# Kernel tuning notes

Hardware: AMD Instinct MI355X
Metric: run time of the kernel (lower is better)

## Reference

```python
import jax, jax.numpy as jnp
import numpy as np
from jax import lax

T, R, W, F_CWT, E, H, HG, NC, K = 16, 200, 50, 32, 128, 256, 256, 2, 20


def _make_wavelets():
    t = np.linspace(-1.0, 1.0, W)
    w0 = 6.0
    freqs = np.linspace(1.0, W / 2.0, F_CWT)
    wr = np.zeros((F_CWT, 1, W), np.float32)
    wi = np.zeros((F_CWT, 1, W), np.float32)
    for i, s in enumerate(freqs):
        norm = s ** (-0.5) * np.pi ** (-0.25)
        ts = t / s
        psi = norm * np.exp(1j * w0 * ts) * np.exp(-0.5 * ts ** 2)
        wr[i, 0] = psi.real.astype(np.float32)
        wi[i, 0] = psi.imag.astype(np.float32)
    return jnp.asarray(wr), jnp.asarray(wi)


def setup_inputs() -> dict:
    key = jax.random.key(0)
    ks = jax.random.split(key, 20)
    wr, wi = _make_wavelets()
    s = 0.05
    inp = {
        "time_windows": jax.random.normal(ks[0], (T, R, W), jnp.float32),
        "wav_real": wr, "wav_imag": wi,
        "conv1_w": jax.random.normal(ks[1], (16, 1, 3, 3), jnp.float32) * s,
        "conv1_b": jnp.zeros((16,), jnp.float32),
        "bn1_g": jnp.ones((16,), jnp.float32), "bn1_b": jnp.zeros((16,), jnp.float32),
        "conv2_w": jax.random.normal(ks[2], (32, 16, 3, 3), jnp.float32) * s,
        "conv2_b": jnp.zeros((32,), jnp.float32),
        "bn2_g": jnp.ones((32,), jnp.float32), "bn2_b": jnp.zeros((32,), jnp.float32),
        "fc_w": jax.random.normal(ks[3], (E, 32), jnp.float32) * s,
        "fc_b": jnp.zeros((E,), jnp.float32),
        "q_w": jax.random.normal(ks[4], (E, E), jnp.float32) * s,
        "q_b": jnp.zeros((E,), jnp.float32),
        "k_w": jax.random.normal(ks[5], (E, E), jnp.float32) * s,
        "k_b": jnp.zeros((E,), jnp.float32),
        "gcn1_w": jax.random.normal(ks[6], (E, H), jnp.float32) * s,
        "gcn1_b": jnp.zeros((H,), jnp.float32),
        "gcn2_w": jax.random.normal(ks[7], (H, H), jnp.float32) * s,
        "gcn2_b": jnp.zeros((H,), jnp.float32),
        "gru_wih": jax.random.normal(ks[8], (3 * HG, H), jnp.float32) * s,
        "gru_whh": jax.random.normal(ks[9], (3 * HG, HG), jnp.float32) * s,
        "gru_bih": jnp.zeros((3 * HG,), jnp.float32),
        "gru_bhh": jnp.zeros((3 * HG,), jnp.float32),
        "cls_w": jax.random.normal(ks[10], (NC, HG), jnp.float32) * s,
        "cls_b": jnp.zeros((NC,), jnp.float32),
    }
    return inp


def _conv_bn_relu_pool(x, w, b, g, beta):
    # conv2d k3 pad1, training-mode BN, relu, maxpool2 (floor)
    x = lax.conv_general_dilated(x, w, (1, 1), ((1, 1), (1, 1)),
                                 dimension_numbers=("NCHW", "OIHW", "NCHW"))
    x = x + b[None, :, None, None]
    mu = x.mean((0, 2, 3), keepdims=True)
    var = x.var((0, 2, 3), keepdims=True)
    x = (x - mu) * lax.rsqrt(var + 1e-5) * g[None, :, None, None] + beta[None, :, None, None]
    x = jax.nn.relu(x)
    return lax.reduce_window(x, -jnp.inf, lax.max, (1, 1, 2, 2), (1, 1, 2, 2), "VALID")


def _forward(time_windows, wav_real, wav_imag, conv1_w, conv1_b, bn1_g, bn1_b,
             conv2_w, conv2_b, bn2_g, bn2_b, fc_w, fc_b, q_w, q_b, k_w, k_b,
             gcn1_w, gcn1_b, gcn2_w, gcn2_b, gru_wih, gru_whh, gru_bih, gru_bhh,
             cls_w, cls_b):
    N = T * R
    x = time_windows.reshape(N, 1, W)
    pl = (W - 1) // 2
    pr = (W - 1) - pl  # torch padding='same' (extra on right)
    re = lax.conv_general_dilated(x, wav_real, (1,), [(pl, pr)],
                                  dimension_numbers=("NCH", "OIH", "NCH"))
    im = lax.conv_general_dilated(x, wav_imag, (1,), [(pl, pr)],
                                  dimension_numbers=("NCH", "OIH", "NCH"))
    scal = jnp.sqrt(re * re + im * im)              # [N, F_CWT, W]

    h = scal[:, None]                               # [N,1,F,W]
    h = _conv_bn_relu_pool(h, conv1_w, conv1_b, bn1_g, bn1_b)
    h = _conv_bn_relu_pool(h, conv2_w, conv2_b, bn2_g, bn2_b)
    pooled = h.mean((2, 3))                         # adaptive avg pool -> [N,32]
    emb = pooled @ fc_w.T + fc_b                    # [N,E]
    emb = emb.reshape(T, R, E)

    # sparse-attention graph generation (per window, vectorized over T)
    Q = emb @ q_w.T + q_b
    Kp = emb @ k_w.T + k_b
    attn = jnp.einsum("tre,tse->trs", Q, Kp) / (E ** 0.5)
    attn = jax.nn.leaky_relu(attn, 0.2)
    _, idx = lax.top_k(attn, K)                     # [T,R,K]
    mask = jnp.zeros_like(attn).at[
        jnp.arange(T)[:, None, None], jnp.arange(R)[None, :, None], idx].set(1.0)
    masked = attn * mask
    masked = jnp.where(masked == 0.0, -1e9, masked)
    adj = jax.nn.softmax(masked, axis=-1)           # [T,R,R] row-stochastic, topk-sparse

    # GCNConv x2 with edge weights (PyG gcn_norm: remaining self-loops weight 1,
    ii = jnp.arange(R)
    diag = adj[:, ii, ii]
    adj_sl = adj.at[:, ii, ii].set(jnp.where(diag == 0.0, 1.0, diag))
    Bm = jnp.swapaxes(adj_sl, 1, 2)
    deg = Bm.sum(-1)
    dinv = jnp.where(deg > 0, deg, 1.0) ** -0.5
    An = dinv[:, :, None] * Bm * dinv[:, None, :]   # [T,R,R]
    g = jax.nn.relu(jnp.einsum("trs,tsh->trh", An, emb @ gcn1_w) + gcn1_b)
    g = jax.nn.relu(jnp.einsum("trs,tsh->trh", An, g @ gcn2_w) + gcn2_b)
    g_emb = g.mean(1)                               # [T,H]

    # GRU over the T graph embeddings (batch 1, gate order r,z,n)
    def step(hprev, xt):
        gi = xt @ gru_wih.T + gru_bih
        gh = hprev @ gru_whh.T + gru_bhh
        ir, iz, inn = jnp.split(gi, 3)
        hr, hz, hn = jnp.split(gh, 3)
        r = jax.nn.sigmoid(ir + hr)
        z = jax.nn.sigmoid(iz + hz)
        n = jnp.tanh(inn + r * hn)
        return (1.0 - z) * n + z * hprev, None

    hT, _ = lax.scan(step, jnp.zeros((HG,), emb.dtype), g_emb)
    pred = (hT @ cls_w.T + cls_b)[None]             # [1,NC]

    edge_var = jnp.mean(jnp.var(adj, axis=0, ddof=1))
    avg_adj = adj.mean(0)[None]                     # [1,R,R]
    return pred, avg_adj, edge_var


def reference(time_windows, wav_real, wav_imag, conv1_w, conv1_b, bn1_g, bn1_b,
              conv2_w, conv2_b, bn2_g, bn2_b, fc_w, fc_b, q_w, q_b, k_w, k_b,
              gcn1_w, gcn1_b, gcn2_w, gcn2_b, gru_wih, gru_whh, gru_bih, gru_bhh,
              cls_w, cls_b):
    return _forward(time_windows, wav_real, wav_imag, conv1_w, conv1_b, bn1_g, bn1_b,
                    conv2_w, conv2_b, bn2_g, bn2_b, fc_w, fc_b, q_w, q_b, k_w, k_b,
                    gcn1_w, gcn1_b, gcn2_w, gcn2_b, gru_wih, gru_whh, gru_bih, gru_bhh,
                    cls_w, cls_b)
```

## Files before the change

### kernel.cpp

```cpp
#include <hip/hip_runtime.h>
#include <cfloat>
#include <cmath>

#define T_ 16
#define R_ 200
#define W_ 50
#define FCWT 32
#define E_ 128
#define K_ 20
#define N_ 3200
#define GRU_BLOCKS 6

__device__ __forceinline__ void waveReduce2(float& a, float& b) {
#pragma unroll
    for (int o = 32; o > 0; o >>= 1) {
        a += __shfl_down(a, o, 64);
        b += __shfl_down(b, o, 64);
    }
}

__global__ __launch_bounds__(256) void cwt_conv1_stats_kernel(const float* __restrict__ x,
                                                              const float* __restrict__ wr,
                                                              const float* __restrict__ wi,
                                                              const float* __restrict__ w1,
                                                              const float* __restrict__ b1,
                                                              float* __restrict__ scal,
                                                              double* __restrict__ psum,
                                                              double* __restrict__ psq) {
    int n = blockIdx.x, tid = threadIdx.x;
    __shared__ float sxp[112];
    __shared__ float swr[FCWT * W_];
    __shared__ float swi[FCWT * W_];
    __shared__ float P1[34 * 52];
    __shared__ float ls[256], lq[256];
    if (tid < 112) sxp[tid] = (tid >= 24 && tid < 74) ? x[n * 50 + (tid - 24)] : 0.f;
    for (int idx = tid; idx < FCWT * W_; idx += 256) { swr[idx] = wr[idx]; swi[idx] = wi[idx]; }
    for (int idx = tid; idx < 34 * 52; idx += 256) P1[idx] = 0.f;
    __syncthreads();
    if (tid < 64) {
        int f = tid >> 1, i0 = (tid & 1) * 25;
        float xw[25], ar[25], ai[25];
#pragma unroll
        for (int d = 0; d < 25; ++d) { xw[d] = sxp[i0 + d]; ar[d] = 0.f; ai[d] = 0.f; }
        const float* wrf = &swr[f * 50];
        const float* wif = &swi[f * 50];
        for (int j = 0; j < 50; ++j) {
            float wrv = wrf[j], wiv = wif[j];
#pragma unroll
            for (int d = 0; d < 25; ++d) { ar[d] += xw[d] * wrv; ai[d] += xw[d] * wiv; }
            float xnew = sxp[i0 + j + 25];
#pragma unroll
            for (int d = 0; d < 24; ++d) xw[d] = xw[d + 1];
            xw[24] = xnew;
        }
#pragma unroll
        for (int d = 0; d < 25; ++d) {
            float v = sqrtf(ar[d] * ar[d] + ai[d] * ai[d]);
            P1[(f + 1) * 52 + (i0 + d + 1)] = v;
        }
    }
    __syncthreads();
    for (int idx = tid; idx < 1600; idx += 256) {
        int ff = idx / 50, ii = idx % 50;
        scal[n * 1600 + idx] = P1[(ff + 1) * 52 + ii + 1];
    }
    int c = tid & 15, pg = tid >> 4;
    float wv[9];
#pragma unroll
    for (int k = 0; k < 9; ++k) wv[k] = w1[c * 9 + k];
    float bias = b1[c];
    const float* r0p = &P1[(2 * pg + 0) * 52];
    const float* r1p = &P1[(2 * pg + 1) * 52];
    const float* r2p = &P1[(2 * pg + 2) * 52];
    const float* r3p = &P1[(2 * pg + 3) * 52];
    float c0[4], c1[4];
    c0[0] = r0p[0]; c0[1] = r1p[0]; c0[2] = r2p[0]; c0[3] = r3p[0];
    c1[0] = r0p[1]; c1[1] = r1p[1]; c1[2] = r2p[1]; c1[3] = r3p[1];
    float s = 0.f, q = 0.f;
    for (int xx = 0; xx < 50; ++xx) {
        float c2[4];
        c2[0] = r0p[xx + 2]; c2[1] = r1p[xx + 2]; c2[2] = r2p[xx + 2]; c2[3] = r3p[xx + 2];
        float v0 = bias + c0[0] * wv[0] + c1[0] * wv[1] + c2[0] * wv[2]
                        + c0[1] * wv[3] + c1[1] * wv[4] + c2[1] * wv[5]
                        + c0[2] * wv[6] + c1[2] * wv[7] + c2[2] * wv[8];
        float v1 = bias + c0[1] * wv[0] + c1[1] * wv[1] + c2[1] * wv[2]
                        + c0[2] * wv[3] + c1[2] * wv[4] + c2[2] * wv[5]
                        + c0[3] * wv[6] + c1[3] * wv[7] + c2[3] * wv[8];
        s += v0 + v1; q += v0 * v0 + v1 * v1;
#pragma unroll
        for (int rr = 0; rr < 4; ++rr) { c0[rr] = c1[rr]; c1[rr] = c2[rr]; }
    }
    ls[tid] = s; lq[tid] = q;
    __syncthreads();
    if (tid < 16) {
        float ss = 0.f, qq = 0.f;
        for (int g = 0; g < 16; ++g) { ss += ls[tid + 16 * g]; qq += lq[tid + 16 * g]; }
        psum[n * 16 + tid] = (double)ss;
        psq[n * 16 + tid] = (double)qq;
    }
}

__global__ __launch_bounds__(256) void bn_finalize_kernel(const double* __restrict__ psum,
                                                          const double* __restrict__ psq,
                                                          const float* __restrict__ g,
                                                          const float* __restrict__ beta,
                                                          float* __restrict__ scale,
                                                          float* __restrict__ shift,
                                                          int C, double inv_count) {
    int c = blockIdx.x, tid = threadIdx.x;
    double s = 0.0, q = 0.0;
    for (int n = tid; n < N_; n += 256) { s += psum[n * C + c]; q += psq[n * C + c]; }
#pragma unroll
    for (int o = 32; o > 0; o >>= 1) { s += __shfl_down(s, o, 64); q += __shfl_down(q, o, 64); }
    __shared__ double sa[4], sb[4];
    int lane = tid & 63, wid = tid >> 6;
    if (lane == 0) { sa[wid] = s; sb[wid] = q; }
    __syncthreads();
    if (tid == 0) {
        s = sa[0] + sa[1] + sa[2] + sa[3];
        q = sb[0] + sb[1] + sb[2] + sb[3];
        double mu = s * inv_count;
        double var = q * inv_count - mu * mu;
        double rstd = 1.0 / sqrt(var + 1e-5);
        double gg = (double)g[c];
        scale[c] = (float)(gg * rstd);
        shift[c] = (float)((double)beta[c] - mu * rstd * gg);
    }
}

__global__ __launch_bounds__(256) void conv1_norm_pool_kernel(const float* __restrict__ scal,
                                                              const float* __restrict__ w1,
                                                              const float* __restrict__ b1,
                                                              const float* __restrict__ scale,
                                                              const float* __restrict__ shift,
                                                              float* __restrict__ pooled1) {
    int n = blockIdx.x, tid = threadIdx.x;
    __shared__ float P1[34 * 52];
    __shared__ float outb[6400];
    for (int idx = tid; idx < 34 * 52; idx += 256) {
        int yy = idx / 52, xx = idx % 52;
        float v = 0.f;
        if (yy >= 1 && yy <= 32 && xx >= 1 && xx <= 50)
            v = scal[n * 1600 + (yy - 1) * 50 + (xx - 1)];
        P1[idx] = v;
    }
    __syncthreads();
    int c = tid & 15, py = tid >> 4;
    float wv[9];
#pragma unroll
    for (int k = 0; k < 9; ++k) wv[k] = w1[c * 9 + k];
    float bias = b1[c], sc = scale[c], sh = shift[c];
    const float* r0p = &P1[(2 * py + 0) * 52];
    const float* r1p = &P1[(2 * py + 1) * 52];
    const float* r2p = &P1[(2 * py + 2) * 52];
    const float* r3p = &P1[(2 * py + 3) * 52];
    float c0[4], c1[4];
    c0[0] = r0p[0]; c0[1] = r1p[0]; c0[2] = r2p[0]; c0[3] = r3p[0];
    c1[0] = r0p[1]; c1[1] = r1p[1]; c1[2] = r2p[1]; c1[3] = r3p[1];
    float pmax = -FLT_MAX;
    for (int xx = 0; xx < 50; ++xx) {
        float c2[4];
        c2[0] = r0p[xx + 2]; c2[1] = r1p[xx + 2]; c2[2] = r2p[xx + 2]; c2[3] = r3p[xx + 2];
        float v0 = bias + c0[0] * wv[0] + c1[0] * wv[1] + c2[0] * wv[2]
                        + c0[1] * wv[3] + c1[1] * wv[4] + c2[1] * wv[5]
                        + c0[2] * wv[6] + c1[2] * wv[7] + c2[2] * wv[8];
        float v1 = bias + c0[1] * wv[0] + c1[1] * wv[1] + c2[1] * wv[2]
                        + c0[2] * wv[3] + c1[2] * wv[4] + c2[2] * wv[5]
                        + c0[3] * wv[6] + c1[3] * wv[7] + c2[3] * wv[8];
        float m2 = fmaxf(v0 * sc + sh, v1 * sc + sh);
        if ((xx & 1) == 0) pmax = m2;
        else outb[(c * 16 + py) * 25 + (xx >> 1)] = fmaxf(fmaxf(pmax, m2), 0.f);
#pragma unroll
        for (int rr = 0; rr < 4; ++rr) { c0[rr] = c1[rr]; c1[rr] = c2[rr]; }
    }
    __syncthreads();
    for (int idx = tid; idx < 6400; idx += 256)
        pooled1[(size_t)n * 6400 + idx] = outb[idx];
}

__global__ __launch_bounds__(256) void conv2_compute_kernel(const float* __restrict__ pooled1,
                                                            const float* __restrict__ w2,
                                                            const float* __restrict__ b2,
                                                            float* __restrict__ mm,
                                                            double* __restrict__ psum,
                                                            double* __restrict__ psq,
                                                            int store_min) {
    int n = blockIdx.x, tid = threadIdx.x;
    __shared__ float P2[16 * 18 * 28];
    __shared__ float swT[144 * 32];
    __shared__ float ls[256], lq[256];
    for (int idx = tid; idx < 16 * 18 * 28; idx += 256) {
        int ci = idx / 504, rem = idx % 504, yy = rem / 28, xx = rem % 28;
        float v = 0.f;
        if (yy >= 1 && yy <= 16 && xx >= 1 && xx <= 25)
            v = pooled1[((size_t)n * 16 + ci) * 400 + (yy - 1) * 25 + (xx - 1)];
        P2[idx] = v;
    }
    for (int idx = tid; idx < 4608; idx += 256) {
        int co = idx / 144, r = idx % 144;
        swT[r * 32 + co] = w2[idx];
    }
    __syncthreads();
    int co = tid & 31, pg = tid >> 5;
    float bias = b2[co];
    float acc0[25], acc1[25];
#pragma unroll
    for (int cv = 0; cv < 25; ++cv) { acc0[cv] = bias; acc1[cv] = bias; }
    for (int ci = 0; ci < 16; ++ci) {
        const float* wb = &swT[ci * 288 + co];
        float w[9];
#pragma unroll
        for (int k = 0; k < 9; ++k) w[k] = wb[k * 32];
        const float* base = &P2[ci * 504 + (2 * pg) * 28];
#pragma unroll
        for (int iy = 0; iy < 4; ++iy) {
            float r[28];
            const float4* rp = (const float4*)(base + iy * 28);
#pragma unroll
            for (int m = 0; m < 7; ++m) {
                float4 v4 = rp[m];
                r[4 * m] = v4.x; r[4 * m + 1] = v4.y; r[4 * m + 2] = v4.z; r[4 * m + 3] = v4.w;
            }
            if (iy < 3) {
                int kb = iy * 3;
#pragma unroll
                for (int cv = 0; cv < 25; ++cv)
                    acc0[cv] += r[cv] * w[kb] + r[cv + 1] * w[kb + 1] + r[cv + 2] * w[kb + 2];
            }
            if (iy >= 1) {
                int kb = (iy - 1) * 3;
#pragma unroll
                for (int cv = 0; cv < 25; ++cv)
                    acc1[cv] += r[cv] * w[kb] + r[cv + 1] * w[kb + 1] + r[cv + 2] * w[kb + 2];
            }
        }
    }
    float s = 0.f, q = 0.f;
#pragma unroll
    for (int cv = 0; cv < 25; ++cv) {
        s += acc0[cv] + acc1[cv];
        q += acc0[cv] * acc0[cv] + acc1[cv] * acc1[cv];
    }
    int stride = store_min ? 64 : 32;
#pragma unroll
    for (int pc = 0; pc < 12; ++pc) {
        float v00 = acc0[2 * pc], v01 = acc0[2 * pc + 1];
        float v10 = acc1[2 * pc], v11 = acc1[2 * pc + 1];
        float mx = fmaxf(fmaxf(v00, v01), fmaxf(v10, v11));
        int cell = pg * 12 + pc;
        mm[((size_t)n * 96 + cell) * stride + co] = mx;
        if (store_min) {
            float mn = fminf(fminf(v00, v01), fminf(v10, v11));
            mm[((size_t)n * 96 + cell) * 64 + 32 + co] = mn;
        }
    }
    ls[tid] = s; lq[tid] = q;
    __syncthreads();
    if (tid < 32) {
        float ss = 0.f, qq = 0.f;
        for (int g2 = 0; g2 < 8; ++g2) { ss += ls[tid + 32 * g2]; qq += lq[tid + 32 * g2]; }
        psum[n * 32 + tid] = (double)ss;
        psq[n * 32 + tid] = (double)qq;
    }
}

__global__ __launch_bounds__(256) void pool_mean_kernel(const float* __restrict__ mm,
                                                        const float* __restrict__ scale,
                                                        const float* __restrict__ shift,
                                                        float* __restrict__ pm,
                                                        int store_min) {
    int n = blockIdx.x, tid = threadIdx.x;
    int co = tid & 31, grp = tid >> 5;
    float sc = scale[co], sh = shift[co];
    int stride = store_min ? 64 : 32;
    float acc = 0.f;
    for (int j = 0; j < 12; ++j) {
        int cell = grp * 12 + j;
        float v;
        if (store_min && sc < 0.f) {
            float mn = mm[((size_t)n * 96 + cell) * 64 + 32 + co];
            v = mn * sc + sh;
        } else {
            float mx = mm[((size_t)n * 96 + cell) * stride + co];
            v = mx * sc + sh;
        }
        acc += fmaxf(v, 0.f);
    }
    __shared__ float red[256];
    red[tid] = acc;
    __syncthreads();
    if (tid < 32) {
        float t = 0.f;
        for (int g = 0; g < 8; ++g) t += red[co + 32 * g];
        pm[n * 32 + co] = t * (1.f / 96.f);
    }
}

__global__ __launch_bounds__(128) void fc_kernel(const float* __restrict__ pm,
                                                 const float* __restrict__ fc_w,
                                                 const float* __restrict__ fc_b,
                                                 float* __restrict__ emb) {
    int n = blockIdx.x, e = threadIdx.x;
    __shared__ float sp[32];
    if (e < 32) sp[e] = pm[n * 32 + e];
    __syncthreads();
    const float* w = fc_w + e * 32;
    float acc = fc_b[e];
    for (int c = 0; c < 32; ++c) acc += sp[c] * w[c];
    emb[n * 128 + e] = acc;
}

__global__ __launch_bounds__(128) void qk_kernel(const float* __restrict__ emb,
                                                 const float* __restrict__ q_w,
                                                 const float* __restrict__ q_b,
                                                 const float* __restrict__ k_w,
                                                 const float* __restrict__ k_b,
                                                 float* __restrict__ Q,
                                                 float* __restrict__ Kp) {
    int n = blockIdx.x, e = threadIdx.x;
    const float* w = (blockIdx.y == 0) ? q_w : k_w;
    const float* b = (blockIdx.y == 0) ? q_b : k_b;
    float* out = (blockIdx.y == 0) ? Q : Kp;
    __shared__ float se[128];
    se[e] = emb[n * 128 + e];
    __syncthreads();
    const float* wr = w + e * 128;
    float acc = b[e];
    for (int k = 0; k < 128; ++k) acc += se[k] * wr[k];
    out[n * 128 + e] = acc;
}

__global__ __launch_bounds__(256) void attn_kernel(const float* __restrict__ Q,
                                                   const float* __restrict__ Kp,
                                                   float* __restrict__ attn) {
    int r = blockIdx.x, t = blockIdx.y, tid = threadIdx.x;
    __shared__ float sq[128];
    if (tid < 128) sq[tid] = Q[(t * 200 + r) * 128 + tid];
    __syncthreads();
    if (tid < 200) {
        const float4* kp4 = (const float4*)(Kp + (size_t)(t * 200 + tid) * 128);
        float acc = 0.f;
#pragma unroll 8
        for (int e4 = 0; e4 < 32; ++e4) {
            float4 k4 = kp4[e4];
            acc += sq[e4 * 4 + 0] * k4.x + sq[e4 * 4 + 1] * k4.y +
                   sq[e4 * 4 + 2] * k4.z + sq[e4 * 4 + 3] * k4.w;
        }
        acc = acc / 11.313708498984761f;
        acc = (acc >= 0.f) ? acc : 0.2f * acc;
        attn[(size_t)(t * 200 + r) * 200 + tid] = acc;
    }
}

__global__ __launch_bounds__(64) void topk_softmax_kernel(const float* __restrict__ attn,
                                                          float* __restrict__ adj) {
    int row = blockIdx.x;
    int lane = threadIdx.x;
    const float* a = attn + (size_t)row * 200;
    float v[4], w[4];
#pragma unroll
    for (int j = 0; j < 4; ++j) {
        int i = lane + 64 * j;
        float x = (i < 200) ? a[i] : -FLT_MAX;
        v[j] = x; w[j] = x;
    }
    unsigned sel = 0;
    for (int it = 0; it < K_; ++it) {
        float best = -FLT_MAX; int bidx = 0x7fffffff;
#pragma unroll
        for (int j = 0; j < 4; ++j) {
            int i = lane + 64 * j;
            if (w[j] > best || (w[j] == best && i < bidx)) { best = w[j]; bidx = i; }
        }
#pragma unroll
        for (int off = 32; off > 0; off >>= 1) {
            float ob = __shfl_down(best, off, 64);
            int oi = __shfl_down(bidx, off, 64);
            if (ob > best || (ob == best && oi < bidx)) { best = ob; bidx = oi; }
        }
        bidx = __shfl(bidx, 0, 64);
        if ((bidx & 63) == lane) { int j = bidx >> 6; w[j] = -FLT_MAX; sel |= (1u << j); }
    }
    float mv[4]; float m = -FLT_MAX;
#pragma unroll
    for (int j = 0; j < 4; ++j) {
        int i = lane + 64 * j;
        float x = -1e9f;
        if (i < 200 && ((sel >> j) & 1u)) x = (v[j] == 0.f) ? -1e9f : v[j];
        mv[j] = x; m = fmaxf(m, x);
    }
#pragma unroll
    for (int off = 32; off > 0; off >>= 1) m = fmaxf(m, __shfl_xor(m, off, 64));
    float s = 0.f; float e[4];
#pragma unroll
    for (int j = 0; j < 4; ++j) {
        int i = lane + 64 * j;
        e[j] = (i < 200) ? expf(mv[j] - m) : 0.f;
        s += e[j];
    }
#pragma unroll
    for (int off = 32; off > 0; off >>= 1) s += __shfl_xor(s, off, 64);
    float inv = 1.f / s;
#pragma unroll
    for (int j = 0; j < 4; ++j) {
        int i = lane + 64 * j;
        if (i < 200) adj[(size_t)row * 200 + i] = e[j] * inv;
    }
}

__global__ __launch_bounds__(256) void deg_kernel(const float* __restrict__ adj,
                                                  float* __restrict__ dinv) {
    int t = blockIdx.x, tid = threadIdx.x;
    if (tid < 200) {
        float acc = 0.f;
        for (int s = 0; s < 200; ++s) {
            float v = adj[(size_t)(t * 200 + s) * 200 + tid];
            if (s == tid) v = (v == 0.f) ? 1.f : v;
            acc += v;
        }
        float d = (acc > 0.f) ? acc : 1.f;
        dinv[t * 200 + tid] = 1.f / sqrtf(d);
    }
}

__global__ __launch_bounds__(256) void an_tile_kernel(const float* __restrict__ adj,
                                                      const float* __restrict__ dinv,
                                                      float* __restrict__ An) {
    int t = blockIdx.y;
    int tr = blockIdx.x >> 2, tc = blockIdx.x & 3;
    int r0 = tr * 50, s0 = tc * 50;
    int tid = threadIdx.x;
    __shared__ float Tt[50 * 51];
    __shared__ float dr[50], ds[50];
    for (int idx = tid; idx < 2500; idx += 256) {
        int a = idx / 50, b = idx % 50;
        Tt[a * 51 + b] = adj[(size_t)(t * 200 + s0 + a) * 200 + r0 + b];
    }
    if (tid < 50) dr[tid] = dinv[t * 200 + r0 + tid];
    else if (tid >= 64 && tid < 114) ds[tid - 64] = dinv[t * 200 + s0 + (tid - 64)];
    __syncthreads();
    for (int idx = tid; idx < 2500; idx += 256) {
        int rl = idx / 50, sl = idx % 50;
        float v = Tt[sl * 51 + rl];
        if (r0 + rl == s0 + sl) v = (v == 0.f) ? 1.f : v;
        An[(size_t)(t * 200 + r0 + rl) * 200 + s0 + sl] = dr[rl] * v * ds[sl];
    }
}

__global__ __launch_bounds__(256) void linear8_kernel(const float* __restrict__ in,
                                                      const float* __restrict__ w,
                                                      float* __restrict__ out, int IN) {
    int n0 = blockIdx.x * 8, h = threadIdx.x;
    __shared__ float sin_[8 * 256];
    for (int idx = h; idx < 8 * IN; idx += 256) sin_[idx] = in[(size_t)n0 * IN + idx];
    __syncthreads();
    float acc[8];
#pragma unroll
    for (int m = 0; m < 8; ++m) acc[m] = 0.f;
    for (int k = 0; k < IN; ++k) {
        float wv = w[k * 256 + h];
#pragma unroll
        for (int m = 0; m < 8; ++m) acc[m] += sin_[m * IN + k] * wv;
    }
#pragma unroll
    for (int m = 0; m < 8; ++m) out[(size_t)(n0 + m) * 256 + h] = acc[m];
}

__global__ __launch_bounds__(256) void gcn_agg_kernel(const float* __restrict__ An,
                                                      const float* __restrict__ X,
                                                      const float* __restrict__ b,
                                                      float* __restrict__ out) {
    int t = blockIdx.y, r0 = blockIdx.x * 8, h = threadIdx.x;
    __shared__ float sa[8 * 200];
    for (int idx = h; idx < 1600; idx += 256)
        sa[idx] = An[(size_t)(t * 200 + r0) * 200 + idx];
    __syncthreads();
    const float* Xt = X + (size_t)t * 200 * 256;
    float acc[8];
#pragma unroll
    for (int m = 0; m < 8; ++m) acc[m] = 0.f;
    for (int s = 0; s < 200; ++s) {
        float xv = Xt[s * 256 + h];
#pragma unroll
        for (int m = 0; m < 8; ++m) acc[m] += sa[m * 200 + s] * xv;
    }
    float bb = b[h];
#pragma unroll
    for (int m = 0; m < 8; ++m)
        out[(size_t)(t * 200 + r0 + m) * 256 + h] = fmaxf(acc[m] + bb, 0.f);
}

__global__ __launch_bounds__(256) void gemb_kernel(const float* __restrict__ g2,
                                                   float* __restrict__ g_emb) {
    int t = blockIdx.x, h = threadIdx.x;
    float acc = 0.f;
    for (int r = 0; r < 200; ++r) acc += g2[(size_t)(t * 200 + r) * 256 + h];
    g_emb[t * 256 + h] = acc * (1.f / 200.f);
}

__global__ __launch_bounds__(256) void transpose_768x256_kernel(const float* __restrict__ in,
                                                                float* __restrict__ outT) {
    int gid = blockIdx.x * 256 + threadIdx.x;
    int k = gid / 768, j = gid % 768;
    outT[gid] = in[j * 256 + k];
}

__global__ __launch_bounds__(768) void gi_kernel(const float* __restrict__ g_emb,
                                                 const float* __restrict__ wihT,
                                                 const float* __restrict__ bih,
                                                 float* __restrict__ GI) {
    int t = blockIdx.x, j = threadIdx.x;
    __shared__ float sg[256];
    if (j < 256) sg[j] = g_emb[t * 256 + j];
    __syncthreads();
    float acc = bih[j];
    for (int k = 0; k < 256; ++k) acc += sg[k] * wihT[k * 768 + j];
    GI[t * 768 + j] = acc;
}

__global__ __launch_bounds__(256) void gru_cls_kernel(const float* __restrict__ GI,
                                                      const float* __restrict__ whhT,
                                                      const float* __restrict__ bhh,
                                                      const float* __restrict__ cls_w,
                                                      const float* __restrict__ cls_b,
                                                      float* __restrict__ GH,
                                                      int* __restrict__ flags,
                                                      float* __restrict__ out) {
    int b = blockIdx.x, tid = threadIdx.x;
    int jl = tid & 127;
    int kc = tid >> 7;
    int j = b * 128 + jl;
    float wreg[128];
#pragma unroll 16
    for (int k = 0; k < 128; ++k)
        wreg[k] = whhT[(size_t)(kc * 128 + k) * 768 + j];
    __shared__ float hcur[256];
    __shared__ float part[256];
    __shared__ float s0[4], s1[4];
    hcur[tid] = 0.f;
    __syncthreads();
    for (int st = 0; st < 16; ++st) {
        float p = 0.f;
        const float* hb = &hcur[kc * 128];
#pragma unroll 16
        for (int k = 0; k < 128; ++k) p += hb[k] * wreg[k];
        part[tid] = p;
        __syncthreads();
        if (tid < 128) {
            GH[st * 768 + b * 128 + tid] = part[tid] + part[tid + 128];
        }
        __threadfence();
        __syncthreads();
        if (tid == 0)
            __hip_atomic_store(&flags[b], st + 1, __ATOMIC_RELEASE, __HIP_MEMORY_SCOPE_AGENT);
        for (int bb = 0; bb < GRU_BLOCKS; ++bb) {
            while (__hip_atomic_load(&flags[bb], __ATOMIC_ACQUIRE, __HIP_MEMORY_SCOPE_AGENT) <= st)
                __builtin_amdgcn_s_sleep(2);
        }
        float ghr = GH[st * 768 + tid]       + bhh[tid];
        float ghz = GH[st * 768 + 256 + tid] + bhh[256 + tid];
        float ghn = GH[st * 768 + 512 + tid] + bhh[512 + tid];
        float gir = GI[st * 768 + tid];
        float giz = GI[st * 768 + 256 + tid];
        float gin = GI[st * 768 + 512 + tid];
        float r = 1.f / (1.f + expf(-(gir + ghr)));
        float z = 1.f / (1.f + expf(-(giz + ghz)));
        float nn = tanhf(gin + r * ghn);
        float hnew = (1.f - z) * nn + z * hcur[tid];
        __syncthreads();
        hcur[tid] = hnew;
        __syncthreads();
    }
    if (b == 0) {
        float v0 = hcur[tid] * cls_w[tid];
        float v1 = hcur[tid] * cls_w[256 + tid];
        waveReduce2(v0, v1);
        int lane = tid & 63, wid = tid >> 6;
        if (lane == 0) { s0[wid] = v0; s1[wid] = v1; }
        __syncthreads();
        if (tid == 0) {
            out[0] = s0[0] + s0[1] + s0[2] + s0[3] + cls_b[0];
            out[1] = s1[0] + s1[1] + s1[2] + s1[3] + cls_b[1];
        }
    }
}

__global__ __launch_bounds__(256) void edge_kernel(const float* __restrict__ adj,
                                                   float* __restrict__ out) {
    int gid = blockIdx.x * 256 + threadIdx.x;
    float var = 0.f;
    if (gid < 40000) {
        float v[16]; float s = 0.f;
#pragma unroll
        for (int t = 0; t < 16; ++t) { v[t] = adj[t * 40000 + gid]; s += v[t]; }
        float mean = s * (1.f / 16.f);
        float q = 0.f;
#pragma unroll
        for (int t = 0; t < 16; ++t) { float d = v[t] - mean; q += d * d; }
        var = q * (1.f / 15.f);
        out[2 + gid] = mean;
    }
    float dummy = 0.f;
    waveReduce2(var, dummy);
    __shared__ float sa[4];
    int lane = threadIdx.x & 63, wid = threadIdx.x >> 6;
    if (lane == 0) sa[wid] = var;
    __syncthreads();
    if (threadIdx.x == 0) {
        float bs = sa[0] + sa[1] + sa[2] + sa[3];
        atomicAdd(&out[40002], bs * (1.f / 40000.f));
    }
}

extern "C" void kernel_launch(void* const* d_in, const int* in_sizes, int n_in,
                              void* d_out, int out_size, void* d_ws, size_t ws_size,
                              hipStream_t stream) {
    const float* tw      = (const float*)d_in[0];
    const float* wav_r   = (const float*)d_in[1];
    const float* wav_i   = (const float*)d_in[2];
    const float* conv1_w = (const float*)d_in[3];
    const float* conv1_b = (const float*)d_in[4];
    const float* bn1_g   = (const float*)d_in[5];
    const float* bn1_b   = (const float*)d_in[6];
    const float* conv2_w = (const float*)d_in[7];
    const float* conv2_b = (const float*)d_in[8];
    const float* bn2_g   = (const float*)d_in[9];
    const float* bn2_b   = (const float*)d_in[10];
    const float* fc_w    = (const float*)d_in[11];
    const float* fc_b    = (const float*)d_in[12];
    const float* q_w     = (const float*)d_in[13];
    const float* q_b     = (const float*)d_in[14];
    const float* k_w     = (const float*)d_in[15];
    const float* k_b     = (const float*)d_in[16];
    const float* gcn1_w  = (const float*)d_in[17];
    const float* gcn1_b  = (const float*)d_in[18];
    const float* gcn2_w  = (const float*)d_in[19];
    const float* gcn2_b  = (const float*)d_in[20];
    const float* gru_wih = (const float*)d_in[21];
    const float* gru_whh = (const float*)d_in[22];
    const float* gru_bih = (const float*)d_in[23];
    const float* gru_bhh = (const float*)d_in[24];
    const float* cls_w   = (const float*)d_in[25];
    const float* cls_b   = (const float*)d_in[26];
    float* out = (float*)d_out;
    (void)in_sizes; (void)n_in; (void)out_size;

    const size_t POOLED1_B = (size_t)N_ * 16 * 16 * 25 * 4;
    const size_t SCALU_B   = (size_t)N_ * 1600 * 4;
    const size_t MM_FULL_B = (size_t)N_ * 96 * 64 * 4;
    const size_t MM_MAX_B  = (size_t)N_ * 96 * 32 * 4;
    const size_t P1S_B     = (size_t)N_ * 16 * 8;
    const size_t P2S_B     = (size_t)N_ * 32 * 8;
    const size_t WT_B      = (size_t)768 * 256 * 4;
    size_t fixed = POOLED1_B + SCALU_B + 2 * P1S_B + 2 * P2S_B + 2 * WT_B + 8 * 256 + 65536;
    int store_min = (ws_size >= fixed + MM_FULL_B) ? 1 : 0;
    const size_t MM_B = store_min ? MM_FULL_B : MM_MAX_B;

    size_t off = 0;
    char* Wb = (char*)d_ws;
    auto take = [&](size_t bytes) -> char* {
        char* p = Wb + off;
        off += (bytes + 255) & ~(size_t)255;
        return p;
    };
    float* pooled1 = (float*)take(POOLED1_B);
    char*  scalU   = take(SCALU_B);
    char*  mmU     = take(MM_B);
    double* p1sum = (double*)take(P1S_B);
    double* p1sq  = (double*)take(P1S_B);
    double* p2sum = (double*)take(P2S_B);
    double* p2sq  = (double*)take(P2S_B);
    float* scale1 = (float*)take(64 * 4);
    float* shift1 = (float*)take(64 * 4);
    float* scale2 = (float*)take(64 * 4);
    float* shift2 = (float*)take(64 * 4);
    float* wihT   = (float*)take(WT_B);
    float* whhT   = (float*)take(WT_B);
    float* dinv   = (float*)take((size_t)T_ * 200 * 4);
    float* GH     = (float*)take((size_t)16 * 768 * 4);
    int*   flags  = (int*)take(256);

    float* scal = (float*)scalU;
    float* pm   = (float*)(scalU + 0);
    float* emb  = (float*)(scalU + 409600);
    float* Q    = (float*)(scalU + 409600 + 1638400);
    float* Kp   = (float*)(scalU + 409600 + 2 * 1638400);

    float* mm   = (float*)mmU;
    size_t moff = 0;
    auto mtake = [&](size_t bytes) -> float* {
        float* p = (float*)(mmU + moff);
        moff += (bytes + 255) & ~(size_t)255;
        return p;
    };
    float* attn  = mtake((size_t)T_ * 200 * 200 * 4);
    float* adj   = mtake((size_t)T_ * 200 * 200 * 4);
    float* An    = mtake((size_t)T_ * 200 * 200 * 4);
    float* X1    = mtake((size_t)N_ * 256 * 4);
    float* g1    = mtake((size_t)N_ * 256 * 4);
    float* X2    = mtake((size_t)N_ * 256 * 4);
    float* g2    = mtake((size_t)N_ * 256 * 4);
    float* g_emb = mtake((size_t)T_ * 256 * 4);
    float* GI    = mtake((size_t)T_ * 768 * 4);

    transpose_768x256_kernel<<<768, 256, 0, stream>>>(gru_wih, wihT);
    transpose_768x256_kernel<<<768, 256, 0, stream>>>(gru_whh, whhT);
    cwt_conv1_stats_kernel<<<N_, 256, 0, stream>>>(tw, wav_r, wav_i, conv1_w, conv1_b,
                                                   scal, p1sum, p1sq);
    bn_finalize_kernel<<<16, 256, 0, stream>>>(p1sum, p1sq, bn1_g, bn1_b, scale1, shift1,
                                               16, 1.0 / 5120000.0);
    conv1_norm_pool_kernel<<<N_, 256, 0, stream>>>(scal, conv1_w, conv1_b, scale1, shift1,
                                                   pooled1);
    conv2_compute_kernel<<<N_, 256, 0, stream>>>(pooled1, conv2_w, conv2_b, mm,
                                                 p2sum, p2sq, store_min);
    bn_finalize_kernel<<<32, 256, 0, stream>>>(p2sum, p2sq, bn2_g, bn2_b, scale2, shift2,
                                               32, 1.0 / 1280000.0);
    pool_mean_kernel<<<N_, 256, 0, stream>>>(mm, scale2, shift2, pm, store_min);
    fc_kernel<<<N_, 128, 0, stream>>>(pm, fc_w, fc_b, emb);
    qk_kernel<<<dim3(N_, 2), 128, 0, stream>>>(emb, q_w, q_b, k_w, k_b, Q, Kp);
    attn_kernel<<<dim3(200, 16), 256, 0, stream>>>(Q, Kp, attn);
    topk_softmax_kernel<<<N_, 64, 0, stream>>>(attn, adj);
    deg_kernel<<<16, 256, 0, stream>>>(adj, dinv);
    an_tile_kernel<<<dim3(16, 16), 256, 0, stream>>>(adj, dinv, An);
    linear8_kernel<<<N_ / 8, 256, 0, stream>>>(emb, gcn1_w, X1, 128);
    gcn_agg_kernel<<<dim3(25, 16), 256, 0, stream>>>(An, X1, gcn1_b, g1);
    linear8_kernel<<<N_ / 8, 256, 0, stream>>>(g1, gcn2_w, X2, 256);
    gcn_agg_kernel<<<dim3(25, 16), 256, 0, stream>>>(An, X2, gcn2_b, g2);
    gemb_kernel<<<16, 256, 0, stream>>>(g2, g_emb);
    gi_kernel<<<16, 768, 0, stream>>>(g_emb, wihT, gru_bih, GI);
    hipMemsetAsync(flags, 0, 256, stream);
    gru_cls_kernel<<<GRU_BLOCKS, 256, 0, stream>>>(GI, whhT, gru_bhh, cls_w, cls_b,
                                                   GH, flags, out);
    hipMemsetAsync(out + 40002, 0, sizeof(float), stream);
    edge_kernel<<<(40000 + 255) / 256, 256, 0, stream>>>(adj, out);
}
```

Before: 865.8 us.

## Fuse small kernels, parallelize CWT over all threads, store padded intermediates

Merges several small launches into fewer kernels: all weight transposes run in one kernel, pool-mean/fc/QK projection become one kernel, attention scores and top-k softmax become one kernel, and the graph-embedding mean is folded into the GRU input projection. The CWT stage now uses all 256 threads with 7 outputs each, where before only 64 threads computed 25 outputs each. Intermediates are stored pre-padded so the next conv kernels can copy them with float4 loads without index math. conv2 gets an occupancy hint in its launch bounds, and the padded buffers increase memory traffic somewhat.

```diff
diff --git a/kernel.cpp b/kernel.cpp
--- a/kernel.cpp
+++ b/kernel.cpp
@@ -19,12 +19,41 @@
     }
 }
 
+__global__ __launch_bounds__(256) void transpose_multi_kernel(const float* __restrict__ wih,
+                                                              const float* __restrict__ whh,
+                                                              const float* __restrict__ qw,
+                                                              const float* __restrict__ kw,
+                                                              const float* __restrict__ fcw,
+                                                              float* __restrict__ wihT,
+                                                              float* __restrict__ whhT,
+                                                              float* __restrict__ qwT,
+                                                              float* __restrict__ kwT,
+                                                              float* __restrict__ fcwT) {
+    int b = blockIdx.x, tid = threadIdx.x;
+    if (b < 768) {
+        int gid = b * 256 + tid; int k = gid / 768, j = gid % 768;
+        wihT[gid] = wih[j * 256 + k];
+    } else if (b < 1536) {
+        int gid = (b - 768) * 256 + tid; int k = gid / 768, j = gid % 768;
+        whhT[gid] = whh[j * 256 + k];
+    } else if (b < 1600) {
+        int gid = (b - 1536) * 256 + tid; int k = gid >> 7, e = gid & 127;
+        qwT[gid] = qw[e * 128 + k];
+    } else if (b < 1664) {
+        int gid = (b - 1600) * 256 + tid; int k = gid >> 7, e = gid & 127;
+        kwT[gid] = kw[e * 128 + k];
+    } else {
+        int gid = (b - 1664) * 256 + tid; int c = gid >> 7, e = gid & 127;
+        fcwT[gid] = fcw[e * 32 + c];
+    }
+}
+
 __global__ __launch_bounds__(256) void cwt_conv1_stats_kernel(const float* __restrict__ x,
                                                               const float* __restrict__ wr,
                                                               const float* __restrict__ wi,
                                                               const float* __restrict__ w1,
                                                               const float* __restrict__ b1,
-                                                              float* __restrict__ scal,
+                                                              float* __restrict__ scalP,
                                                               double* __restrict__ psum,
                                                               double* __restrict__ psq) {
     int n = blockIdx.x, tid = threadIdx.x;
@@ -37,33 +66,29 @@
     for (int idx = tid; idx < FCWT * W_; idx += 256) { swr[idx] = wr[idx]; swi[idx] = wi[idx]; }
     for (int idx = tid; idx < 34 * 52; idx += 256) P1[idx] = 0.f;
     __syncthreads();
-    if (tid < 64) {
-        int f = tid >> 1, i0 = (tid & 1) * 25;
-        float xw[25], ar[25], ai[25];
-#pragma unroll
-        for (int d = 0; d < 25; ++d) { xw[d] = sxp[i0 + d]; ar[d] = 0.f; ai[d] = 0.f; }
+    {
+        int f = tid >> 3, cg = tid & 7, i0 = cg * 7;
+        float xw[7], ar[7], ai[7];
+#pragma unroll
+        for (int d = 0; d < 7; ++d) { xw[d] = sxp[i0 + d]; ar[d] = 0.f; ai[d] = 0.f; }
         const float* wrf = &swr[f * 50];
         const float* wif = &swi[f * 50];
         for (int j = 0; j < 50; ++j) {
             float wrv = wrf[j], wiv = wif[j];
 #pragma unroll
-            for (int d = 0; d < 25; ++d) { ar[d] += xw[d] * wrv; ai[d] += xw[d] * wiv; }
-            float xnew = sxp[i0 + j + 25];
-#pragma unroll
-            for (int d = 0; d < 24; ++d) xw[d] = xw[d + 1];
-            xw[24] = xnew;
-        }
-#pragma unroll
-        for (int d = 0; d < 25; ++d) {
-            float v = sqrtf(ar[d] * ar[d] + ai[d] * ai[d]);
-            P1[(f + 1) * 52 + (i0 + d + 1)] = v;
-        }
-    }
-    __syncthreads();
-    for (int idx = tid; idx < 1600; idx += 256) {
-        int ff = idx / 50, ii = idx % 50;
-        scal[n * 1600 + idx] = P1[(ff + 1) * 52 + ii + 1];
-    }
+            for (int d = 0; d < 7; ++d) { ar[d] += xw[d] * wrv; ai[d] += xw[d] * wiv; }
+#pragma unroll
+            for (int d = 0; d < 6; ++d) xw[d] = xw[d + 1];
+            xw[6] = sxp[i0 + j + 7];
+        }
+#pragma unroll
+        for (int d = 0; d < 7; ++d) {
+            int i = i0 + d;
+            if (i < 50) P1[(f + 1) * 52 + i + 1] = sqrtf(ar[d] * ar[d] + ai[d] * ai[d]);
+        }
+    }
+    __syncthreads();
+    for (int idx = tid; idx < 34 * 52; idx += 256) scalP[(size_t)n * 1768 + idx] = P1[idx];
     int c = tid & 15, pg = tid >> 4;
     float wv[9];
 #pragma unroll
@@ -128,7 +153,7 @@
     }
 }
 
-__global__ __launch_bounds__(256) void conv1_norm_pool_kernel(const float* __restrict__ scal,
+__global__ __launch_bounds__(256) void conv1_norm_pool_kernel(const float* __restrict__ scalP,
                                                               const float* __restrict__ w1,
                                                               const float* __restrict__ b1,
                                                               const float* __restrict__ scale,
@@ -136,14 +161,9 @@
                                                               float* __restrict__ pooled1) {
     int n = blockIdx.x, tid = threadIdx.x;
     __shared__ float P1[34 * 52];
-    __shared__ float outb[6400];
-    for (int idx = tid; idx < 34 * 52; idx += 256) {
-        int yy = idx / 52, xx = idx % 52;
-        float v = 0.f;
-        if (yy >= 1 && yy <= 32 && xx >= 1 && xx <= 50)
-            v = scal[n * 1600 + (yy - 1) * 50 + (xx - 1)];
-        P1[idx] = v;
-    }
+    __shared__ float outb[16 * 18 * 28];
+    for (int idx = tid; idx < 34 * 52; idx += 256) P1[idx] = scalP[(size_t)n * 1768 + idx];
+    for (int idx = tid; idx < 16 * 18 * 28; idx += 256) outb[idx] = 0.f;
     __syncthreads();
     int c = tid & 15, py = tid >> 4;
     float wv[9];
@@ -169,32 +189,31 @@
                         + c0[3] * wv[6] + c1[3] * wv[7] + c2[3] * wv[8];
         float m2 = fmaxf(v0 * sc + sh, v1 * sc + sh);
         if ((xx & 1) == 0) pmax = m2;
-        else outb[(c * 16 + py) * 25 + (xx >> 1)] = fmaxf(fmaxf(pmax, m2), 0.f);
+        else outb[(c * 18 + py + 1) * 28 + ((xx >> 1) + 1)] = fmaxf(fmaxf(pmax, m2), 0.f);
 #pragma unroll
         for (int rr = 0; rr < 4; ++rr) { c0[rr] = c1[rr]; c1[rr] = c2[rr]; }
     }
     __syncthreads();
-    for (int idx = tid; idx < 6400; idx += 256)
-        pooled1[(size_t)n * 6400 + idx] = outb[idx];
-}
-
-__global__ __launch_bounds__(256) void conv2_compute_kernel(const float* __restrict__ pooled1,
-                                                            const float* __restrict__ w2,
-                                                            const float* __restrict__ b2,
-                                                            float* __restrict__ mm,
-                                                            double* __restrict__ psum,
-                                                            double* __restrict__ psq,
-                                                            int store_min) {
+    const float4* ob4 = (const float4*)outb;
+    float4* p4 = (float4*)(pooled1 + (size_t)n * 8064);
+    for (int idx = tid; idx < 2016; idx += 256) p4[idx] = ob4[idx];
+}
+
+__global__ __launch_bounds__(256, 3) void conv2_compute_kernel(const float* __restrict__ pooled1,
+                                                               const float* __restrict__ w2,
+                                                               const float* __restrict__ b2,
+                                                               float* __restrict__ mm,
+                                                               double* __restrict__ psum,
+                                                               double* __restrict__ psq,
+                                                               int store_min) {
     int n = blockIdx.x, tid = threadIdx.x;
     __shared__ float P2[16 * 18 * 28];
     __shared__ float swT[144 * 32];
     __shared__ float ls[256], lq[256];
-    for (int idx = tid; idx < 16 * 18 * 28; idx += 256) {
-        int ci = idx / 504, rem = idx % 504, yy = rem / 28, xx = rem % 28;
-        float v = 0.f;
-        if (yy >= 1 && yy <= 16 && xx >= 1 && xx <= 25)
-            v = pooled1[((size_t)n * 16 + ci) * 400 + (yy - 1) * 25 + (xx - 1)];
-        P2[idx] = v;
+    {
+        const float4* src4 = (const float4*)(pooled1 + (size_t)n * 8064);
+        float4* dst4 = (float4*)P2;
+        for (int idx = tid; idx < 2016; idx += 256) dst4[idx] = src4[idx];
     }
     for (int idx = tid; idx < 4608; idx += 256) {
         int co = idx / 144, r = idx % 144;
@@ -264,13 +283,24 @@
     }
 }
 
-__global__ __launch_bounds__(256) void pool_mean_kernel(const float* __restrict__ mm,
-                                                        const float* __restrict__ scale,
-                                                        const float* __restrict__ shift,
-                                                        float* __restrict__ pm,
-                                                        int store_min) {
+__global__ __launch_bounds__(256) void pm_fc_qk_kernel(const float* __restrict__ mm,
+                                                       const float* __restrict__ scale,
+                                                       const float* __restrict__ shift,
+                                                       const float* __restrict__ fcwT,
+                                                       const float* __restrict__ fc_b,
+                                                       const float* __restrict__ qwT,
+                                                       const float* __restrict__ q_b,
+                                                       const float* __restrict__ kwT,
+                                                       const float* __restrict__ k_b,
+                                                       float* __restrict__ emb,
+                                                       float* __restrict__ Q,
+                                                       float* __restrict__ Kp,
+                                                       int store_min) {
     int n = blockIdx.x, tid = threadIdx.x;
     int co = tid & 31, grp = tid >> 5;
+    __shared__ float red[256];
+    __shared__ float pm_s[32];
+    __shared__ float se[128];
     float sc = scale[co], sh = shift[co];
     int stride = store_min ? 64 : 32;
     float acc = 0.f;
@@ -286,56 +316,39 @@
         }
         acc += fmaxf(v, 0.f);
     }
-    __shared__ float red[256];
     red[tid] = acc;
     __syncthreads();
     if (tid < 32) {
         float t = 0.f;
         for (int g = 0; g < 8; ++g) t += red[co + 32 * g];
-        pm[n * 32 + co] = t * (1.f / 96.f);
-    }
-}
-
-__global__ __launch_bounds__(128) void fc_kernel(const float* __restrict__ pm,
-                                                 const float* __restrict__ fc_w,
-                                                 const float* __restrict__ fc_b,
-                                                 float* __restrict__ emb) {
-    int n = blockIdx.x, e = threadIdx.x;
-    __shared__ float sp[32];
-    if (e < 32) sp[e] = pm[n * 32 + e];
-    __syncthreads();
-    const float* w = fc_w + e * 32;
-    float acc = fc_b[e];
-    for (int c = 0; c < 32; ++c) acc += sp[c] * w[c];
-    emb[n * 128 + e] = acc;
-}
-
-__global__ __launch_bounds__(128) void qk_kernel(const float* __restrict__ emb,
-                                                 const float* __restrict__ q_w,
-                                                 const float* __restrict__ q_b,
-                                                 const float* __restrict__ k_w,
-                                                 const float* __restrict__ k_b,
-                                                 float* __restrict__ Q,
-                                                 float* __restrict__ Kp) {
-    int n = blockIdx.x, e = threadIdx.x;
-    const float* w = (blockIdx.y == 0) ? q_w : k_w;
-    const float* b = (blockIdx.y == 0) ? q_b : k_b;
-    float* out = (blockIdx.y == 0) ? Q : Kp;
-    __shared__ float se[128];
-    se[e] = emb[n * 128 + e];
-    __syncthreads();
-    const float* wr = w + e * 128;
-    float acc = b[e];
-    for (int k = 0; k < 128; ++k) acc += se[k] * wr[k];
-    out[n * 128 + e] = acc;
-}
-
-__global__ __launch_bounds__(256) void attn_kernel(const float* __restrict__ Q,
-                                                   const float* __restrict__ Kp,
-                                                   float* __restrict__ attn) {
+        pm_s[tid] = t * (1.f / 96.f);
+    }
+    __syncthreads();
+    if (tid < 128) {
+        float a = fc_b[tid];
+        for (int c = 0; c < 32; ++c) a += pm_s[c] * fcwT[c * 128 + tid];
+        se[tid] = a;
+        emb[(size_t)n * 128 + tid] = a;
+    }
+    __syncthreads();
+    {
+        int e = tid & 127, half = tid >> 7;
+        const float* w = half ? kwT : qwT;
+        float b = half ? k_b[e] : q_b[e];
+        float a = b;
+        for (int k = 0; k < 128; ++k) a += se[k] * w[k * 128 + e];
+        if (half) Kp[(size_t)n * 128 + e] = a;
+        else      Q[(size_t)n * 128 + e] = a;
+    }
+}
+
+__global__ __launch_bounds__(256) void attn_topk_kernel(const float* __restrict__ Q,
+                                                        const float* __restrict__ Kp,
+                                                        float* __restrict__ adj) {
     int r = blockIdx.x, t = blockIdx.y, tid = threadIdx.x;
     __shared__ float sq[128];
-    if (tid < 128) sq[tid] = Q[(t * 200 + r) * 128 + tid];
+    __shared__ float sc[200];
+    if (tid < 128) sq[tid] = Q[(size_t)(t * 200 + r) * 128 + tid];
     __syncthreads();
     if (tid < 200) {
         const float4* kp4 = (const float4*)(Kp + (size_t)(t * 200 + tid) * 128);
@@ -347,64 +360,61 @@
                    sq[e4 * 4 + 2] * k4.z + sq[e4 * 4 + 3] * k4.w;
         }
         acc = acc / 11.313708498984761f;
-        acc = (acc >= 0.f) ? acc : 0.2f * acc;
-        attn[(size_t)(t * 200 + r) * 200 + tid] = acc;
-    }
-}
-
-__global__ __launch_bounds__(64) void topk_softmax_kernel(const float* __restrict__ attn,
-                                                          float* __restrict__ adj) {
-    int row = blockIdx.x;
-    int lane = threadIdx.x;
-    const float* a = attn + (size_t)row * 200;
-    float v[4], w[4];
-#pragma unroll
-    for (int j = 0; j < 4; ++j) {
-        int i = lane + 64 * j;
-        float x = (i < 200) ? a[i] : -FLT_MAX;
-        v[j] = x; w[j] = x;
-    }
-    unsigned sel = 0;
-    for (int it = 0; it < K_; ++it) {
-        float best = -FLT_MAX; int bidx = 0x7fffffff;
+        sc[tid] = (acc >= 0.f) ? acc : 0.2f * acc;
+    }
+    __syncthreads();
+    if (tid < 64) {
+        int lane = tid;
+        float v[4], w[4];
 #pragma unroll
         for (int j = 0; j < 4; ++j) {
             int i = lane + 64 * j;
-            if (w[j] > best || (w[j] == best && i < bidx)) { best = w[j]; bidx = i; }
-        }
-#pragma unroll
-        for (int off = 32; off > 0; off >>= 1) {
-            float ob = __shfl_down(best, off, 64);
-            int oi = __shfl_down(bidx, off, 64);
-            if (ob > best || (ob == best && oi < bidx)) { best = ob; bidx = oi; }
-        }
-        bidx = __shfl(bidx, 0, 64);
-        if ((bidx & 63) == lane) { int j = bidx >> 6; w[j] = -FLT_MAX; sel |= (1u << j); }
-    }
-    float mv[4]; float m = -FLT_MAX;
-#pragma unroll
-    for (int j = 0; j < 4; ++j) {
-        int i = lane + 64 * j;
-        float x = -1e9f;
-        if (i < 200 && ((sel >> j) & 1u)) x = (v[j] == 0.f) ? -1e9f : v[j];
-        mv[j] = x; m = fmaxf(m, x);
-    }
-#pragma unroll
-    for (int off = 32; off > 0; off >>= 1) m = fmaxf(m, __shfl_xor(m, off, 64));
-    float s = 0.f; float e[4];
-#pragma unroll
-    for (int j = 0; j < 4; ++j) {
-        int i = lane + 64 * j;
-        e[j] = (i < 200) ? expf(mv[j] - m) : 0.f;
-        s += e[j];
-    }
-#pragma unroll
-    for (int off = 32; off > 0; off >>= 1) s += __shfl_xor(s, off, 64);
-    float inv = 1.f / s;
-#pragma unroll
-    for (int j = 0; j < 4; ++j) {
-        int i = lane + 64 * j;
-        if (i < 200) adj[(size_t)row * 200 + i] = e[j] * inv;
+            float x = (i < 200) ? sc[i] : -FLT_MAX;
+            v[j] = x; w[j] = x;
+        }
+        unsigned sel = 0;
+        for (int it = 0; it < K_; ++it) {
+            float best = -FLT_MAX; int bidx = 0x7fffffff;
+#pragma unroll
+            for (int j = 0; j < 4; ++j) {
+                int i = lane + 64 * j;
+                if (w[j] > best || (w[j] == best && i < bidx)) { best = w[j]; bidx = i; }
+            }
+#pragma unroll
+            for (int off = 32; off > 0; off >>= 1) {
+                float ob = __shfl_down(best, off, 64);
+                int oi = __shfl_down(bidx, off, 64);
+                if (ob > best || (ob == best && oi < bidx)) { best = ob; bidx = oi; }
+            }
+            bidx = __shfl(bidx, 0, 64);
+            if ((bidx & 63) == lane) { int j = bidx >> 6; w[j] = -FLT_MAX; sel |= (1u << j); }
+        }
+        float mv[4]; float m = -FLT_MAX;
+#pragma unroll
+        for (int j = 0; j < 4; ++j) {
+            int i = lane + 64 * j;
+            float x = -1e9f;
+            if (i < 200 && ((sel >> j) & 1u)) x = (v[j] == 0.f) ? -1e9f : v[j];
+            mv[j] = x; m = fmaxf(m, x);
+        }
+#pragma unroll
+        for (int off = 32; off > 0; off >>= 1) m = fmaxf(m, __shfl_xor(m, off, 64));
+        float s = 0.f; float e[4];
+#pragma unroll
+        for (int j = 0; j < 4; ++j) {
+            int i = lane + 64 * j;
+            e[j] = (i < 200) ? expf(mv[j] - m) : 0.f;
+            s += e[j];
+        }
+#pragma unroll
+        for (int off = 32; off > 0; off >>= 1) s += __shfl_xor(s, off, 64);
+        float inv = 1.f / s;
+        size_t rowo = (size_t)(t * 200 + r) * 200;
+#pragma unroll
+        for (int j = 0; j < 4; ++j) {
+            int i = lane + 64 * j;
+            if (i < 200) adj[rowo + i] = e[j] * inv;
+        }
     }
 }
 
@@ -490,32 +500,23 @@
         out[(size_t)(t * 200 + r0 + m) * 256 + h] = fmaxf(acc[m] + bb, 0.f);
 }
 
-__global__ __launch_bounds__(256) void gemb_kernel(const float* __restrict__ g2,
-                                                   float* __restrict__ g_emb) {
-    int t = blockIdx.x, h = threadIdx.x;
-    float acc = 0.f;
-    for (int r = 0; r < 200; ++r) acc += g2[(size_t)(t * 200 + r) * 256 + h];
-    g_emb[t * 256 + h] = acc * (1.f / 200.f);
-}
-
-__global__ __launch_bounds__(256) void transpose_768x256_kernel(const float* __restrict__ in,
-                                                                float* __restrict__ outT) {
-    int gid = blockIdx.x * 256 + threadIdx.x;
-    int k = gid / 768, j = gid % 768;
-    outT[gid] = in[j * 256 + k];
-}
-
-__global__ __launch_bounds__(768) void gi_kernel(const float* __restrict__ g_emb,
-                                                 const float* __restrict__ wihT,
-                                                 const float* __restrict__ bih,
-                                                 float* __restrict__ GI) {
-    int t = blockIdx.x, j = threadIdx.x;
+__global__ __launch_bounds__(256) void gemb_gi_kernel(const float* __restrict__ g2,
+                                                      const float* __restrict__ wihT,
+                                                      const float* __restrict__ bih,
+                                                      float* __restrict__ GI) {
+    int t = blockIdx.x, tid = threadIdx.x;
     __shared__ float sg[256];
-    if (j < 256) sg[j] = g_emb[t * 256 + j];
-    __syncthreads();
-    float acc = bih[j];
-    for (int k = 0; k < 256; ++k) acc += sg[k] * wihT[k * 768 + j];
-    GI[t * 768 + j] = acc;
+    {
+        float acc = 0.f;
+        for (int r = 0; r < 200; ++r) acc += g2[(size_t)(t * 200 + r) * 256 + tid];
+        sg[tid] = acc * (1.f / 200.f);
+    }
+    __syncthreads();
+    for (int j = tid; j < 768; j += 256) {
+        float acc = bih[j];
+        for (int k = 0; k < 256; ++k) acc += sg[k] * wihT[k * 768 + j];
+        GI[t * 768 + j] = acc;
+    }
 }
 
 __global__ __launch_bounds__(256) void gru_cls_kernel(const float* __restrict__ GI,
@@ -645,14 +646,14 @@
     float* out = (float*)d_out;
     (void)in_sizes; (void)n_in; (void)out_size;
 
-    const size_t POOLED1_B = (size_t)N_ * 16 * 16 * 25 * 4;
-    const size_t SCALU_B   = (size_t)N_ * 1600 * 4;
+    const size_t POOLED1_B = (size_t)N_ * 8064 * 4;
+    const size_t SCALU_B   = (size_t)N_ * 1768 * 4;
     const size_t MM_FULL_B = (size_t)N_ * 96 * 64 * 4;
     const size_t MM_MAX_B  = (size_t)N_ * 96 * 32 * 4;
     const size_t P1S_B     = (size_t)N_ * 16 * 8;
     const size_t P2S_B     = (size_t)N_ * 32 * 8;
     const size_t WT_B      = (size_t)768 * 256 * 4;
-    size_t fixed = POOLED1_B + SCALU_B + 2 * P1S_B + 2 * P2S_B + 2 * WT_B + 8 * 256 + 65536;
+    size_t fixed = POOLED1_B + SCALU_B + 2 * P1S_B + 2 * P2S_B + 2 * WT_B + 200000 + 262144;
     int store_min = (ws_size >= fixed + MM_FULL_B) ? 1 : 0;
     const size_t MM_B = store_min ? MM_FULL_B : MM_MAX_B;
 
@@ -676,15 +677,17 @@
     float* shift2 = (float*)take(64 * 4);
     float* wihT   = (float*)take(WT_B);
     float* whhT   = (float*)take(WT_B);
+    float* qwT    = (float*)take(128 * 128 * 4);
+    float* kwT    = (float*)take(128 * 128 * 4);
+    float* fcwT   = (float*)take(32 * 128 * 4);
     float* dinv   = (float*)take((size_t)T_ * 200 * 4);
     float* GH     = (float*)take((size_t)16 * 768 * 4);
     int*   flags  = (int*)take(256);
 
-    float* scal = (float*)scalU;
-    float* pm   = (float*)(scalU + 0);
-    float* emb  = (float*)(scalU + 409600);
-    float* Q    = (float*)(scalU + 409600 + 1638400);
-    float* Kp   = (float*)(scalU + 409600 + 2 * 1638400);
+    float* scalP = (float*)scalU;
+    float* emb   = (float*)(scalU + 0);
+    float* Q     = (float*)(scalU + 1638400);
+    float* Kp    = (float*)(scalU + 2 * 1638400);
 
     float* mm   = (float*)mmU;
     size_t moff = 0;
@@ -693,41 +696,36 @@
         moff += (bytes + 255) & ~(size_t)255;
         return p;
     };
-    float* attn  = mtake((size_t)T_ * 200 * 200 * 4);
     float* adj   = mtake((size_t)T_ * 200 * 200 * 4);
     float* An    = mtake((size_t)T_ * 200 * 200 * 4);
     float* X1    = mtake((size_t)N_ * 256 * 4);
     float* g1    = mtake((size_t)N_ * 256 * 4);
     float* X2    = mtake((size_t)N_ * 256 * 4);
     float* g2    = mtake((size_t)N_ * 256 * 4);
-    float* g_emb = mtake((size_t)T_ * 256 * 4);
     float* GI    = mtake((size_t)T_ * 768 * 4);
 
-    transpose_768x256_kernel<<<768, 256, 0, stream>>>(gru_wih, wihT);
-    transpose_768x256_kernel<<<768, 256, 0, stream>>>(gru_whh, whhT);
+    transpose_multi_kernel<<<1680, 256, 0, stream>>>(gru_wih, gru_whh, q_w, k_w, fc_w,
+                                                     wihT, whhT, qwT, kwT, fcwT);
     cwt_conv1_stats_kernel<<<N_, 256, 0, stream>>>(tw, wav_r, wav_i, conv1_w, conv1_b,
-                                                   scal, p1sum, p1sq);
+                                                   scalP, p1sum, p1sq);
     bn_finalize_kernel<<<16, 256, 0, stream>>>(p1sum, p1sq, bn1_g, bn1_b, scale1, shift1,
                                                16, 1.0 / 5120000.0);
-    conv1_norm_pool_kernel<<<N_, 256, 0, stream>>>(scal, conv1_w, conv1_b, scale1, shift1,
+    conv1_norm_pool_kernel<<<N_, 256, 0, stream>>>(scalP, conv1_w, conv1_b, scale1, shift1,
                                                    pooled1);
     conv2_compute_kernel<<<N_, 256, 0, stream>>>(pooled1, conv2_w, conv2_b, mm,
                                                  p2sum, p2sq, store_min);
     bn_finalize_kernel<<<32, 256, 0, stream>>>(p2sum, p2sq, bn2_g, bn2_b, scale2, shift2,
                                                32, 1.0 / 1280000.0);
-    pool_mean_kernel<<<N_, 256, 0, stream>>>(mm, scale2, shift2, pm, store_min);
-    fc_kernel<<<N_, 128, 0, stream>>>(pm, fc_w, fc_b, emb);
-    qk_kernel<<<dim3(N_, 2), 128, 0, stream>>>(emb, q_w, q_b, k_w, k_b, Q, Kp);
-    attn_kernel<<<dim3(200, 16), 256, 0, stream>>>(Q, Kp, attn);
-    topk_softmax_kernel<<<N_, 64, 0, stream>>>(attn, adj);
+    pm_fc_qk_kernel<<<N_, 256, 0, stream>>>(mm, scale2, shift2, fcwT, fc_b,
+                                            qwT, q_b, kwT, k_b, emb, Q, Kp, store_min);
+    attn_topk_kernel<<<dim3(200, 16), 256, 0, stream>>>(Q, Kp, adj);
     deg_kernel<<<16, 256, 0, stream>>>(adj, dinv);
     an_tile_kernel<<<dim3(16, 16), 256, 0, stream>>>(adj, dinv, An);
     linear8_kernel<<<N_ / 8, 256, 0, stream>>>(emb, gcn1_w, X1, 128);
     gcn_agg_kernel<<<dim3(25, 16), 256, 0, stream>>>(An, X1, gcn1_b, g1);
     linear8_kernel<<<N_ / 8, 256, 0, stream>>>(g1, gcn2_w, X2, 256);
     gcn_agg_kernel<<<dim3(25, 16), 256, 0, stream>>>(An, X2, gcn2_b, g2);
-    gemb_kernel<<<16, 256, 0, stream>>>(g2, g_emb);
-    gi_kernel<<<16, 768, 0, stream>>>(g_emb, wihT, gru_bih, GI);
+    gemb_gi_kernel<<<16, 256, 0, stream>>>(g2, wihT, gru_bih, GI);
     hipMemsetAsync(flags, 0, 256, stream);
     gru_cls_kernel<<<GRU_BLOCKS, 256, 0, stream>>>(GI, whhT, gru_bhh, cls_w, cls_b,
                                                    GH, flags, out);
```

After: 924.4 us. 6.8% more time.
